# Kernel tuning notes

Hardware: AMD Instinct MI355X
Metric: run time of the kernel (lower is better)

Reference implementation:

```python
import jax, jax.numpy as jnp
import numpy as np
import math

IN_F = 256
OUT_F = 256
HEADS = 4
HEAD_DIM = OUT_F // HEADS
B, N = 4, 2048


def setup_inputs() -> dict:
    key = jax.random.key(0)
    ks = jax.random.split(key, 7)
    s = 1.0 / math.sqrt(IN_F)
    h = jax.random.normal(ks[0], (B, N, IN_F), dtype=jnp.float32)
    adj = jax.random.randint(ks[1], (N, N), 0, 2, dtype=jnp.int32)
    Wq = jax.random.uniform(ks[2], (IN_F, OUT_F), jnp.float32, -s, s)
    Wk = jax.random.uniform(ks[3], (IN_F, OUT_F), jnp.float32, -s, s)
    Wv = jax.random.uniform(ks[4], (IN_F, OUT_F), jnp.float32, -s, s)
    Wo = jax.random.uniform(ks[5], (OUT_F, OUT_F), jnp.float32, -s, s)
    bo = jax.random.uniform(ks[6], (OUT_F,), jnp.float32, -s, s)
    return {"h": h, "adj": adj, "Wq": Wq, "Wk": Wk, "Wv": Wv, "Wo": Wo, "bo": bo}


def reference(h, adj, Wq, Wk, Wv, Wo, bo):
    Bv, Nv, _ = h.shape
    # project and split heads: [B, H, N, Dh]
    q = (h @ Wq).reshape(Bv, Nv, HEADS, HEAD_DIM).transpose(0, 2, 1, 3)
    k = (h @ Wk).reshape(Bv, Nv, HEADS, HEAD_DIM).transpose(0, 2, 1, 3)
    v = (h @ Wv).reshape(Bv, Nv, HEADS, HEAD_DIM).transpose(0, 2, 1, 3)
    scores = jnp.einsum('bhnd,bhmd->bhnm', q, k) / math.sqrt(HEAD_DIM)
    mask = (adj == 0)[None, None, :, :]  # [1,1,N,N]
    scores = jnp.where(mask, jnp.float32(-1e9), scores)
    attn = jax.nn.softmax(scores, axis=-1)  # dropout is identity in eval / p=0
    out = jnp.einsum('bhnm,bhmd->bhnd', attn, v)
    out = out.transpose(0, 2, 1, 3).reshape(Bv, Nv, OUT_F)
    return h + out @ Wo + bo
```

## Files before the change

### kernel.cpp

```cpp
#include <hip/hip_runtime.h>
#include <hip/hip_bf16.h>

#define B_ 4
#define N_ 2048
#define F_ 256
#define H_ 4
#define D_ 64

typedef __attribute__((ext_vector_type(8))) short short8;
typedef __attribute__((ext_vector_type(4))) float f32x4;
typedef __attribute__((ext_vector_type(4))) unsigned u32x4;

__device__ __forceinline__ unsigned short f2bf(float x) {
  unsigned u = __builtin_bit_cast(unsigned, x);
  u = (u + 0x7fffu + ((u >> 16) & 1u)) >> 16;
  return (unsigned short)u;
}

__device__ __forceinline__ float bf2f(unsigned short x) {
  unsigned u = ((unsigned)x) << 16;
  return __builtin_bit_cast(float, u);
}

__device__ __forceinline__ f32x4 mfma16(short8 a, short8 b, f32x4 c) {
  return __builtin_amdgcn_mfma_f32_16x16x32_bf16(a, b, c, 0, 0, 0);
}

#define QSCALE 0.1803368801111204f

__global__ __launch_bounds__(256) void prep_kernel(
    const float* __restrict__ h, const int* __restrict__ adj,
    const float* __restrict__ Wq, const float* __restrict__ Wk,
    const float* __restrict__ Wv, const float* __restrict__ Wo,
    unsigned short* __restrict__ hbf,
    unsigned short* __restrict__ wqt, unsigned short* __restrict__ wkt,
    unsigned short* __restrict__ wvt, unsigned short* __restrict__ wot,
    unsigned* __restrict__ adjt) {
  int bid = blockIdx.x;
  int tid = threadIdx.x;
  if (bid < 2048) {
    int idx = (bid * 256 + tid) * 4;
    float4 v = *(const float4*)(h + idx);
    ushort4 o;
    o.x = f2bf(v.x); o.y = f2bf(v.y); o.z = f2bf(v.z); o.w = f2bf(v.w);
    *(ushort4*)(hbf + idx) = o;
  } else if (bid < 3072) {
    int t = (bid - 2048) * 256 + tid;
    int w = t >> 16;
    int e = t & 65535;
    int i = e >> 8;
    int o = e & 255;
    const float* W = (w == 0) ? Wq : (w == 1) ? Wk : (w == 2) ? Wv : Wo;
    unsigned short* Wt = (w == 0) ? wqt : (w == 1) ? wkt : (w == 2) ? wvt : wot;
    Wt[o * 256 + i] = f2bf(W[i * 256 + o]);
  } else {
    int lane = tid & 63;
    int wid = (bid - 3072) * 4 + (tid >> 6);
    #pragma unroll
    for (int it = 0; it < 16; ++it) {
      int widx = wid * 16 + it;
      int n = widx >> 5;
      int mw64 = widx & 31;
      unsigned long long m = __ballot(adj[widx * 64 + lane] != 0);
      if (lane == 0) {
        adjt[(2 * mw64) * 2048 + n] = (unsigned)m;
        adjt[(2 * mw64 + 1) * 2048 + n] = (unsigned)(m >> 32);
      }
    }
  }
}

__global__ __launch_bounds__(256) void qkv_gemm(
    const unsigned short* __restrict__ hbf,
    const unsigned short* __restrict__ wqt, const unsigned short* __restrict__ wkt,
    const unsigned short* __restrict__ wvt,
    unsigned short* __restrict__ qb, unsigned short* __restrict__ kb,
    unsigned short* __restrict__ vtb) {
  __shared__ __align__(16) unsigned short blds[64 * 264];
  int lane = threadIdx.x & 63;
  int wv = threadIdx.x >> 6;
  int g = lane >> 4;
  int c = lane & 15;
  int row32 = blockIdx.x * 128 + wv * 32;
  int colbase = blockIdx.y * 64;
  int which = colbase >> 8;
  int fbase = colbase & 255;
  const unsigned short* wt = (which == 0) ? wqt : (which == 1) ? wkt : wvt;

  for (int i = threadIdx.x; i < 64 * 32; i += 256) {
    int col = i >> 5;
    int kc = (i & 31) * 8;
    *(short8*)(blds + col * 264 + kc) = *(const short8*)(wt + (fbase + col) * 256 + kc);
  }
  __syncthreads();

  f32x4 acc[2][4];
  #pragma unroll
  for (int rt = 0; rt < 2; ++rt)
    #pragma unroll
    for (int cc = 0; cc < 4; ++cc) acc[rt][cc] = (f32x4){0.f, 0.f, 0.f, 0.f};

  for (int k = 0; k < 256; k += 32) {
    short8 a[2], b[4];
    #pragma unroll
    for (int rt = 0; rt < 2; ++rt)
      a[rt] = *(const short8*)(hbf + (row32 + rt * 16 + c) * 256 + k + g * 8);
    #pragma unroll
    for (int cc = 0; cc < 4; ++cc)
      b[cc] = *(const short8*)(blds + (cc * 16 + c) * 264 + k + g * 8);
    #pragma unroll
    for (int rt = 0; rt < 2; ++rt)
      #pragma unroll
      for (int cc = 0; cc < 4; ++cc)
        acc[rt][cc] = mfma16(a[rt], b[cc], acc[rt][cc]);
  }

  #pragma unroll
  for (int rt = 0; rt < 2; ++rt) {
    #pragma unroll
    for (int cc = 0; cc < 4; ++cc) {
      #pragma unroll
      for (int r = 0; r < 4; ++r) {
        int row = row32 + rt * 16 + g * 4 + r;
        int f = fbase + cc * 16 + c;
        int hh = f >> 6, d = f & 63;
        int bb = row >> 11, n = row & 2047;
        float v = acc[rt][cc][r];
        if (which == 0)
          qb[((bb * H_ + hh) * N_ + n) * D_ + d] = f2bf(v * QSCALE);
        else if (which == 1)
          kb[((bb * H_ + hh) * N_ + n) * D_ + d] = f2bf(v);
        else
          vtb[((bb * H_ + hh) * D_ + d) * N_ + n] = f2bf(v);
      }
    }
  }
}

__global__ __launch_bounds__(256) void attn_kernel(
    const unsigned short* __restrict__ qb, const unsigned short* __restrict__ kb,
    const unsigned short* __restrict__ vtb, const unsigned* __restrict__ adjt,
    unsigned short* __restrict__ Opart, float* __restrict__ Lp) {
  __shared__ __align__(16) unsigned short plds[4][2][32 * 40];
  int lane = threadIdx.x & 63;
  int wv = threadIdx.x >> 6;
  int g = lane >> 4;
  int c = lane & 15;
  int lb = (blockIdx.x & 7) * 256 + (blockIdx.x >> 3);
  int bh = lb >> 7;
  int rem = lb & 127;
  int qt = rem >> 1;
  int s = (rem & 1) * 4 + wv;
  int task = (bh * 64 + qt) * 8 + s;
  int qbase = qt * 32;
  const unsigned short* Qp = qb + bh * (N_ * D_);
  const unsigned short* Kp = kb + bh * (N_ * D_);
  const unsigned short* Vt = vtb + bh * (D_ * N_);

  short8 qf[2][2];
  #pragma unroll
  for (int rt = 0; rt < 2; ++rt)
    #pragma unroll
    for (int dh = 0; dh < 2; ++dh)
      qf[rt][dh] = *(const short8*)(Qp + (qbase + rt * 16 + c) * D_ + dh * 32 + g * 8);

  f32x4 O[2][4];
  float Lsum[2][4];
  #pragma unroll
  for (int rt = 0; rt < 2; ++rt) {
    #pragma unroll
    for (int dt = 0; dt < 4; ++dt) O[rt][dt] = (f32x4){0.f, 0.f, 0.f, 0.f};
    #pragma unroll
    for (int r = 0; r < 4; ++r) Lsum[rt][r] = 0.f;
  }

  const f32x4 z4 = {0.f, 0.f, 0.f, 0.f};
  int kv0 = s * 256;

  short8 kfa[2][2], kfb[2][2];
  #pragma unroll
  for (int mt = 0; mt < 2; ++mt)
    #pragma unroll
    for (int dh = 0; dh < 2; ++dh)
      kfa[mt][dh] = *(const short8*)(Kp + (kv0 + mt * 16 + c) * D_ + dh * 32 + g * 8);

  for (int it = 0; it < 8; ++it) {
    int mb = kv0 + it * 32;
    int mw = mb >> 5;
    int nmb = (it == 7) ? kv0 : (mb + 32);
    short8 vf[4];
    #pragma unroll
    for (int dt = 0; dt < 4; ++dt)
      vf[dt] = *(const short8*)(Vt + (dt * 16 + c) * N_ + mb + g * 8);
    #pragma unroll
    for (int mt = 0; mt < 2; ++mt)
      #pragma unroll
      for (int dh = 0; dh < 2; ++dh)
        kfb[mt][dh] = *(const short8*)(Kp + (nmb + mt * 16 + c) * D_ + dh * 32 + g * 8);
    u32x4 awq[2];
    #pragma unroll
    for (int rt = 0; rt < 2; ++rt)
      awq[rt] = *(const u32x4*)(adjt + mw * 2048 + qbase + rt * 16 + g * 4);

    __builtin_amdgcn_s_setprio(1);
    f32x4 S[2][2];
    #pragma unroll
    for (int rt = 0; rt < 2; ++rt)
      #pragma unroll
      for (int mt = 0; mt < 2; ++mt) {
        f32x4 ss = mfma16(qf[rt][0], kfa[mt][0], z4);
        S[rt][mt] = mfma16(qf[rt][1], kfa[mt][1], ss);
      }
    __builtin_amdgcn_s_setprio(0);

    unsigned short* myp = plds[wv][it & 1];
    #pragma unroll
    for (int rt = 0; rt < 2; ++rt) {
      #pragma unroll
      for (int r = 0; r < 4; ++r) {
        unsigned aw = awq[rt][r];
        float e0 = __builtin_amdgcn_exp2f(S[rt][0][r]);
        float e1 = __builtin_amdgcn_exp2f(S[rt][1][r]);
        float p0 = ((aw >> c) & 1u) ? e0 : 0.f;
        float p1 = ((aw >> (c + 16)) & 1u) ? e1 : 0.f;
        Lsum[rt][r] += p0 + p1;
        unsigned pr;
        asm("v_cvt_pk_bf16_f32 %0, %1, %2" : "=v"(pr) : "v"(p0), "v"(p1));
        int prow = rt * 16 + g * 4 + r;
        myp[prow * 40 + c] = (unsigned short)pr;
        myp[prow * 40 + 16 + c] = (unsigned short)(pr >> 16);
      }
    }

    short8 pa[2];
    #pragma unroll
    for (int rt = 0; rt < 2; ++rt)
      pa[rt] = *(const short8*)(myp + (rt * 16 + c) * 40 + g * 8);

    __builtin_amdgcn_s_setprio(1);
    #pragma unroll
    for (int dt = 0; dt < 4; ++dt) {
      #pragma unroll
      for (int rt = 0; rt < 2; ++rt)
        O[rt][dt] = mfma16(pa[rt], vf[dt], O[rt][dt]);
    }
    __builtin_amdgcn_s_setprio(0);

    #pragma unroll
    for (int mt = 0; mt < 2; ++mt)
      #pragma unroll
      for (int dh = 0; dh < 2; ++dh)
        kfa[mt][dh] = kfb[mt][dh];
  }

  unsigned short* Ob = Opart + (size_t)task * 2048;
  #pragma unroll
  for (int rt = 0; rt < 2; ++rt) {
    #pragma unroll
    for (int r = 0; r < 4; ++r) {
      float l = Lsum[rt][r];
      l += __shfl_xor(l, 1);
      l += __shfl_xor(l, 2);
      l += __shfl_xor(l, 4);
      l += __shfl_xor(l, 8);
      int row = rt * 16 + g * 4 + r;
      if (c == 0) Lp[task * 32 + row] = l;
      #pragma unroll
      for (int dt = 0; dt < 4; ++dt)
        Ob[row * 64 + dt * 16 + c] = f2bf(O[rt][dt][r]);
    }
  }
}

__global__ __launch_bounds__(256) void combine_kernel(
    const unsigned short* __restrict__ Opart, const float* __restrict__ Lp,
    unsigned short* __restrict__ ao) {
  int t = blockIdx.x * 256 + threadIdx.x;
  int dq = t & 3;
  int n = (t >> 2) & 2047;
  int bh = t >> 13;
  int qt = n >> 5, row32 = n & 31;
  int tbase = bh * 512 + qt * 8;

  float Lg = 0.f;
  #pragma unroll
  for (int s = 0; s < 8; ++s) Lg += Lp[(tbase + s) * 32 + row32];
  float inv = 1.0f / Lg;

  float o[16];
  #pragma unroll
  for (int d = 0; d < 16; ++d) o[d] = 0.f;
  #pragma unroll
  for (int s = 0; s < 8; ++s) {
    const unsigned short* p = Opart + (size_t)(tbase + s) * 2048 + row32 * 64 + dq * 16;
    short8 v0 = *(const short8*)(p);
    short8 v1 = *(const short8*)(p + 8);
    #pragma unroll
    for (int d = 0; d < 8; ++d) {
      o[d]     += bf2f((unsigned short)v0[d]);
      o[8 + d] += bf2f((unsigned short)v1[d]);
    }
  }

  int bb = bh >> 2, hh = bh & 3;
  short8 ob0, ob1;
  #pragma unroll
  for (int d = 0; d < 8; ++d) {
    ob0[d] = (short)f2bf(o[d] * inv);
    ob1[d] = (short)f2bf(o[8 + d] * inv);
  }
  unsigned short* dst = ao + ((size_t)(bb * N_ + n)) * F_ + hh * 64 + dq * 16;
  *(short8*)(dst) = ob0;
  *(short8*)(dst + 8) = ob1;
}

__global__ __launch_bounds__(256) void out_gemm(
    const unsigned short* __restrict__ ao, const unsigned short* __restrict__ wot,
    const float* __restrict__ h, const float* __restrict__ bo,
    float* __restrict__ out) {
  __shared__ __align__(16) unsigned short blds[64 * 264];
  int lane = threadIdx.x & 63;
  int wv = threadIdx.x >> 6;
  int g = lane >> 4;
  int c = lane & 15;
  int row16 = blockIdx.x * 64 + wv * 16;
  int colb = blockIdx.y * 64;
  int arow = row16 + c;

  for (int i = threadIdx.x; i < 64 * 32; i += 256) {
    int col = i >> 5;
    int kc = (i & 31) * 8;
    *(short8*)(blds + col * 264 + kc) = *(const short8*)(wot + (colb + col) * 256 + kc);
  }
  __syncthreads();

  f32x4 acc[4];
  #pragma unroll
  for (int cc = 0; cc < 4; ++cc) acc[cc] = (f32x4){0.f, 0.f, 0.f, 0.f};

  for (int k = 0; k < 256; k += 32) {
    short8 a = *(const short8*)(ao + arow * 256 + k + g * 8);
    #pragma unroll
    for (int cc = 0; cc < 4; ++cc) {
      short8 bfrag = *(const short8*)(blds + (cc * 16 + c) * 264 + k + g * 8);
      acc[cc] = mfma16(a, bfrag, acc[cc]);
    }
  }

  #pragma unroll
  for (int cc = 0; cc < 4; ++cc) {
    #pragma unroll
    for (int r = 0; r < 4; ++r) {
      int row = row16 + g * 4 + r;
      int col = colb + cc * 16 + c;
      out[row * 256 + col] = h[row * 256 + col] + bo[col] + acc[cc][r];
    }
  }
}

extern "C" void kernel_launch(void* const* d_in, const int* in_sizes, int n_in,
                              void* d_out, int out_size, void* d_ws, size_t ws_size,
                              hipStream_t stream) {
  (void)in_sizes; (void)n_in; (void)out_size; (void)ws_size;
  const float* h  = (const float*)d_in[0];
  const int* adj  = (const int*)d_in[1];
  const float* Wq = (const float*)d_in[2];
  const float* Wk = (const float*)d_in[3];
  const float* Wv = (const float*)d_in[4];
  const float* Wo = (const float*)d_in[5];
  const float* bo = (const float*)d_in[6];
  float* out = (float*)d_out;

  char* ws = (char*)d_ws;
  unsigned short* hbf = (unsigned short*)(ws + 0);
  unsigned short* wqt = (unsigned short*)(ws + 4194304);
  unsigned short* wkt = (unsigned short*)(ws + 4325376);
  unsigned short* wvt = (unsigned short*)(ws + 4456448);
  unsigned short* wot = (unsigned short*)(ws + 4587520);
  unsigned*       adjt = (unsigned*)(ws + 4718592);
  unsigned short* qb  = (unsigned short*)(ws + 5242880);
  unsigned short* kb  = (unsigned short*)(ws + 9437184);
  unsigned short* vtb = (unsigned short*)(ws + 13631488);
  unsigned short* ao  = (unsigned short*)(ws + 17825792);
  unsigned short* Opart = (unsigned short*)(ws + 22020096);
  float*          Lp  = (float*)(ws + 55574528);

  prep_kernel<<<4096, 256, 0, stream>>>(h, adj, Wq, Wk, Wv, Wo,
                                        hbf, wqt, wkt, wvt, wot, adjt);
  qkv_gemm<<<dim3(64, 12), 256, 0, stream>>>(hbf, wqt, wkt, wvt, qb, kb, vtb);
  attn_kernel<<<2048, 256, 0, stream>>>(qb, kb, vtb, adjt, Opart, Lp);
  combine_kernel<<<512, 256, 0, stream>>>(Opart, Lp, ao);
  out_gemm<<<dim3(128, 4), 256, 0, stream>>>(ao, wot, h, bo, out);
}
```

Measured before the change: 187.0 us.

## Compute transposed scores so P stays in registers, permute V layout to match

Swaps the MFMA operands to compute S^T, so each lane holds the probability values it needs directly as the A-operand of the PV MFMA. This removes the per-iteration LDS round trip for P. The V^T store in the projection kernel is permuted within 32-token blocks to match the new key ordering in registers. The adjacency mask load and the row-sum reduction are reworked to fit the transposed fragment layout, which costs a permuted scattered store in the projection kernel.

```diff
diff --git a/kernel.cpp b/kernel.cpp
--- a/kernel.cpp
+++ b/kernel.cpp
@@ -9,7 +9,6 @@
 
 typedef __attribute__((ext_vector_type(8))) short short8;
 typedef __attribute__((ext_vector_type(4))) float f32x4;
-typedef __attribute__((ext_vector_type(4))) unsigned u32x4;
 
 __device__ __forceinline__ unsigned short f2bf(float x) {
   unsigned u = __builtin_bit_cast(unsigned, x);
@@ -130,8 +129,11 @@
           qb[((bb * H_ + hh) * N_ + n) * D_ + d] = f2bf(v * QSCALE);
         else if (which == 1)
           kb[((bb * H_ + hh) * N_ + n) * D_ + d] = f2bf(v);
-        else
-          vtb[((bb * H_ + hh) * D_ + d) * N_ + n] = f2bf(v);
+        else {
+          int nn = n & 31;
+          int pos = ((nn >> 2) & 3) * 8 + (nn >> 4) * 4 + (nn & 3);
+          vtb[((bb * H_ + hh) * D_ + d) * N_ + (n & ~31) + pos] = f2bf(v);
+        }
       }
     }
   }
@@ -141,7 +143,6 @@
     const unsigned short* __restrict__ qb, const unsigned short* __restrict__ kb,
     const unsigned short* __restrict__ vtb, const unsigned* __restrict__ adjt,
     unsigned short* __restrict__ Opart, float* __restrict__ Lp) {
-  __shared__ __align__(16) unsigned short plds[4][2][32 * 40];
   int lane = threadIdx.x & 63;
   int wv = threadIdx.x >> 6;
   int g = lane >> 4;
@@ -165,14 +166,11 @@
       qf[rt][dh] = *(const short8*)(Qp + (qbase + rt * 16 + c) * D_ + dh * 32 + g * 8);
 
   f32x4 O[2][4];
-  float Lsum[2][4];
-  #pragma unroll
-  for (int rt = 0; rt < 2; ++rt) {
+  float Lsum[2] = {0.f, 0.f};
+  #pragma unroll
+  for (int rt = 0; rt < 2; ++rt)
     #pragma unroll
     for (int dt = 0; dt < 4; ++dt) O[rt][dt] = (f32x4){0.f, 0.f, 0.f, 0.f};
-    #pragma unroll
-    for (int r = 0; r < 4; ++r) Lsum[rt][r] = 0.f;
-  }
 
   const f32x4 z4 = {0.f, 0.f, 0.f, 0.f};
   int kv0 = s * 256;
@@ -197,53 +195,50 @@
       #pragma unroll
       for (int dh = 0; dh < 2; ++dh)
         kfb[mt][dh] = *(const short8*)(Kp + (nmb + mt * 16 + c) * D_ + dh * 32 + g * 8);
-    u32x4 awq[2];
+    unsigned awr[2];
+    awr[0] = adjt[mw * 2048 + qbase + c] >> (g * 4);
+    awr[1] = adjt[mw * 2048 + qbase + 16 + c] >> (g * 4);
+
+    __builtin_amdgcn_s_setprio(1);
+    f32x4 ST[2][2];
     #pragma unroll
     for (int rt = 0; rt < 2; ++rt)
-      awq[rt] = *(const u32x4*)(adjt + mw * 2048 + qbase + rt * 16 + g * 4);
-
-    __builtin_amdgcn_s_setprio(1);
-    f32x4 S[2][2];
-    #pragma unroll
-    for (int rt = 0; rt < 2; ++rt)
       #pragma unroll
       for (int mt = 0; mt < 2; ++mt) {
-        f32x4 ss = mfma16(qf[rt][0], kfa[mt][0], z4);
-        S[rt][mt] = mfma16(qf[rt][1], kfa[mt][1], ss);
+        f32x4 ss = mfma16(kfa[mt][0], qf[rt][0], z4);
+        ST[rt][mt] = mfma16(kfa[mt][1], qf[rt][1], ss);
       }
     __builtin_amdgcn_s_setprio(0);
 
-    unsigned short* myp = plds[wv][it & 1];
+    short8 pa[2];
     #pragma unroll
     for (int rt = 0; rt < 2; ++rt) {
-      #pragma unroll
-      for (int r = 0; r < 4; ++r) {
-        unsigned aw = awq[rt][r];
-        float e0 = __builtin_amdgcn_exp2f(S[rt][0][r]);
-        float e1 = __builtin_amdgcn_exp2f(S[rt][1][r]);
-        float p0 = ((aw >> c) & 1u) ? e0 : 0.f;
-        float p1 = ((aw >> (c + 16)) & 1u) ? e1 : 0.f;
-        Lsum[rt][r] += p0 + p1;
+      float p[8];
+      #pragma unroll
+      for (int mt = 0; mt < 2; ++mt)
+        #pragma unroll
+        for (int r = 0; r < 4; ++r) {
+          float e = __builtin_amdgcn_exp2f(ST[rt][mt][r]);
+          float pv = ((awr[rt] >> (mt * 16 + r)) & 1u) ? e : 0.f;
+          p[mt * 4 + r] = pv;
+          Lsum[rt] += pv;
+        }
+      union { unsigned u[4]; short8 s8; } pk;
+      #pragma unroll
+      for (int w = 0; w < 4; ++w) {
         unsigned pr;
-        asm("v_cvt_pk_bf16_f32 %0, %1, %2" : "=v"(pr) : "v"(p0), "v"(p1));
-        int prow = rt * 16 + g * 4 + r;
-        myp[prow * 40 + c] = (unsigned short)pr;
-        myp[prow * 40 + 16 + c] = (unsigned short)(pr >> 16);
+        asm("v_cvt_pk_bf16_f32 %0, %1, %2" : "=v"(pr) : "v"(p[w * 2]), "v"(p[w * 2 + 1]));
+        pk.u[w] = pr;
       }
-    }
-
-    short8 pa[2];
-    #pragma unroll
-    for (int rt = 0; rt < 2; ++rt)
-      pa[rt] = *(const short8*)(myp + (rt * 16 + c) * 40 + g * 8);
+      pa[rt] = pk.s8;
+    }
 
     __builtin_amdgcn_s_setprio(1);
     #pragma unroll
-    for (int dt = 0; dt < 4; ++dt) {
+    for (int dt = 0; dt < 4; ++dt)
       #pragma unroll
       for (int rt = 0; rt < 2; ++rt)
         O[rt][dt] = mfma16(pa[rt], vf[dt], O[rt][dt]);
-    }
     __builtin_amdgcn_s_setprio(0);
 
     #pragma unroll
@@ -253,23 +248,23 @@
         kfa[mt][dh] = kfb[mt][dh];
   }
 
+  #pragma unroll
+  for (int rt = 0; rt < 2; ++rt) {
+    float l = Lsum[rt];
+    l += __shfl_xor(l, 16);
+    l += __shfl_xor(l, 32);
+    if (lane < 16) Lp[task * 32 + rt * 16 + c] = l;
+  }
   unsigned short* Ob = Opart + (size_t)task * 2048;
   #pragma unroll
-  for (int rt = 0; rt < 2; ++rt) {
+  for (int rt = 0; rt < 2; ++rt)
     #pragma unroll
     for (int r = 0; r < 4; ++r) {
-      float l = Lsum[rt][r];
-      l += __shfl_xor(l, 1);
-      l += __shfl_xor(l, 2);
-      l += __shfl_xor(l, 4);
-      l += __shfl_xor(l, 8);
       int row = rt * 16 + g * 4 + r;
-      if (c == 0) Lp[task * 32 + row] = l;
       #pragma unroll
       for (int dt = 0; dt < 4; ++dt)
         Ob[row * 64 + dt * 16 + c] = f2bf(O[rt][dt][r]);
     }
-  }
 }
 
 __global__ __launch_bounds__(256) void combine_kernel(
```

Result: faster. 181.5 us (-2.9%).
